# Kernel optimization log

Measured on AMD Instinct MI355X. Metric: run time of the kernel, lower is better.

The kernel has to match this reference:

```python
import jax, jax.numpy as jnp
import numpy as np


def setup_inputs() -> dict:
    key = jax.random.key(0)
    kx, kz = jax.random.split(key)
    B, H, W = 4, 512, 2048
    x = jax.random.normal(kx, (B, 1, H, W), dtype=jnp.float32)
    z = jax.random.uniform(kz, (B, 1, H, W), dtype=jnp.float32)
    return {"x": x, "z": z, "w_ceil": 16}


def reference(x, z, w_ceil):
    # The two structured sparse conv2d's reduce exactly to:
    #   z_exp[b,i,h,j] = z[b,0,h,j-i]            (eye_filter: right-shift, zero pad)
    #   out[b,i,h,j]   = (x*z_exp)[b,i,h,j+i]    (delay kernel + slice: left-shift, zero pad)
    # => out[b,i,h,j] = x[b,0,h,j+i] * z[b,0,h,j], zero where j+i >= W.
    B, _, H, W = x.shape
    shifts = jnp.arange(w_ceil)                       # [w]
    idx = jnp.arange(W)[None, :] + shifts[:, None]    # [w, W], value j+i
    valid = (idx < W)[None, :, None, :]               # [1, w, 1, W]
    idx = jnp.minimum(idx, W - 1)                     # clamp, masked below
    xg = jnp.take(x[:, 0], idx, axis=-1)              # [B, H, w, W]
    xg = jnp.transpose(xg, (0, 2, 1, 3))              # [B, w, H, W]
    out = jnp.where(valid, xg * z, jnp.zeros((), x.dtype))  # z broadcasts over channel dim
    return out
```

## Files before the change

kernel.cpp:

```cpp
#include <hip/hip_runtime.h>


#define B_ 4
#define H_ 512
#define W_ 2048
#define WC_ 16

__global__ __launch_bounds__(256) void
space2features_kernel(const float* __restrict__ x,
                      const float* __restrict__ z,
                      float* __restrict__ out) {
    const int blk = blockIdx.x;
    const int h = blk & (H_ - 1);
    const int i = (blk >> 9) & (WC_ - 1);
    const int b = blk >> 13;

    const size_t inrow = ((size_t)(b * H_ + h)) * W_;
    const float* __restrict__ xr = x + inrow;
    const float* __restrict__ zr = z + inrow;
    float* __restrict__ orow = out + (size_t)blk * W_;

    const int t = threadIdx.x;
    const int ibase = i & ~3;
    const int r = i & 3;
    const bool last_row = (b == B_ - 1) && (h == H_ - 1);

#pragma unroll
    for (int half = 0; half < 2; ++half) {
        const int j = half * 1024 + t * 4;
        const float4 z4 = *(const float4*)(zr + j);
        const int ji = j + i;

        float w0, w1, w2, w3;
        if (!last_row) {
            const float4 A = *(const float4*)(xr + j + ibase);
            const float4 Bv = *(const float4*)(xr + j + ibase + 4);
            switch (r) {
                case 0:  w0 = A.x; w1 = A.y; w2 = A.z; w3 = A.w; break;
                case 1:  w0 = A.y; w1 = A.z; w2 = A.w; w3 = Bv.x; break;
                case 2:  w0 = A.z; w1 = A.w; w2 = Bv.x; w3 = Bv.y; break;
                default: w0 = A.w; w1 = Bv.x; w2 = Bv.y; w3 = Bv.z; break;
            }
        } else {
            w0 = xr[min(ji + 0, W_ - 1)];
            w1 = xr[min(ji + 1, W_ - 1)];
            w2 = xr[min(ji + 2, W_ - 1)];
            w3 = xr[min(ji + 3, W_ - 1)];
        }

        float4 o;
        o.x = (ji + 0 < W_) ? w0 * z4.x : 0.0f;
        o.y = (ji + 1 < W_) ? w1 * z4.y : 0.0f;
        o.z = (ji + 2 < W_) ? w2 * z4.z : 0.0f;
        o.w = (ji + 3 < W_) ? w3 * z4.w : 0.0f;
        *(float4*)(orow + j) = o;
    }
}

extern "C" void kernel_launch(void* const* d_in, const int* in_sizes, int n_in,
                              void* d_out, int out_size, void* d_ws, size_t ws_size,
                              hipStream_t stream) {
    const float* x = (const float*)d_in[0];
    const float* z = (const float*)d_in[1];
    float* out = (float*)d_out;

    const int grid = B_ * WC_ * H_;
    space2features_kernel<<<grid, 256, 0, stream>>>(x, z, out);
}
```

Measured before the change: 290.0 us.

## Stage x row in LDS and emit all 16 shifts per block

Each block now handles one (b,h) row. It loads x and z once, stages x in shared memory with a zero-padded tail, and writes all 16 shifted output channels from registers. This removes the 16x redundant global reads of x and z and the per-block shift switch, and zero padding replaces the bounds masks. The grid shrinks 16x, which may cut parallelism and latency hiding. Each thread also issues 16 strided stores.

```diff
diff --git a/kernel.cpp b/kernel.cpp
--- a/kernel.cpp
+++ b/kernel.cpp
@@ -10,50 +10,50 @@
 space2features_kernel(const float* __restrict__ x,
                       const float* __restrict__ z,
                       float* __restrict__ out) {
+    __shared__ float xs[W_ + 20];
+
     const int blk = blockIdx.x;
     const int h = blk & (H_ - 1);
-    const int i = (blk >> 9) & (WC_ - 1);
-    const int b = blk >> 13;
+    const int b = blk >> 9;
 
-    const size_t inrow = ((size_t)(b * H_ + h)) * W_;
+    const size_t inrow = (size_t)blk * W_;
     const float* __restrict__ xr = x + inrow;
     const float* __restrict__ zr = z + inrow;
-    float* __restrict__ orow = out + (size_t)blk * W_;
 
     const int t = threadIdx.x;
-    const int ibase = i & ~3;
-    const int r = i & 3;
-    const bool last_row = (b == B_ - 1) && (h == H_ - 1);
+
+    float4 zv[2];
+#pragma unroll
+    for (int half = 0; half < 2; ++half) {
+        const int j = half * 1024 + t * 4;
+        const float4 x4 = *(const float4*)(xr + j);
+        zv[half] = *(const float4*)(zr + j);
+        *(float4*)(xs + j) = x4;
+    }
+    if (t < 20) xs[W_ + t] = 0.0f;
+    __syncthreads();
+
+    float* __restrict__ obase = out + ((size_t)(b * WC_) * H_ + h) * W_;
 
 #pragma unroll
     for (int half = 0; half < 2; ++half) {
         const int j = half * 1024 + t * 4;
-        const float4 z4 = *(const float4*)(zr + j);
-        const int ji = j + i;
 
-        float w0, w1, w2, w3;
-        if (!last_row) {
-            const float4 A = *(const float4*)(xr + j + ibase);
-            const float4 Bv = *(const float4*)(xr + j + ibase + 4);
-            switch (r) {
-                case 0:  w0 = A.x; w1 = A.y; w2 = A.z; w3 = A.w; break;
-                case 1:  w0 = A.y; w1 = A.z; w2 = A.w; w3 = Bv.x; break;
-                case 2:  w0 = A.z; w1 = A.w; w2 = Bv.x; w3 = Bv.y; break;
-                default: w0 = A.w; w1 = Bv.x; w2 = Bv.y; w3 = Bv.z; break;
-            }
-        } else {
-            w0 = xr[min(ji + 0, W_ - 1)];
-            w1 = xr[min(ji + 1, W_ - 1)];
-            w2 = xr[min(ji + 2, W_ - 1)];
-            w3 = xr[min(ji + 3, W_ - 1)];
+        float xv[20];
+#pragma unroll
+        for (int g = 0; g < 5; ++g)
+            *(float4*)(xv + 4 * g) = *(const float4*)(xs + j + 4 * g);
+
+        const float4 z4 = zv[half];
+#pragma unroll
+        for (int i = 0; i < WC_; ++i) {
+            float4 o;
+            o.x = xv[i + 0] * z4.x;
+            o.y = xv[i + 1] * z4.y;
+            o.z = xv[i + 2] * z4.z;
+            o.w = xv[i + 3] * z4.w;
+            *(float4*)(obase + (size_t)i * (H_ * W_) + j) = o;
         }
-
-        float4 o;
-        o.x = (ji + 0 < W_) ? w0 * z4.x : 0.0f;
-        o.y = (ji + 1 < W_) ? w1 * z4.y : 0.0f;
-        o.z = (ji + 2 < W_) ? w2 * z4.z : 0.0f;
-        o.w = (ji + 3 < W_) ? w3 * z4.w : 0.0f;
-        *(float4*)(orow + j) = o;
     }
 }
 
@@ -64,6 +64,6 @@
     const float* z = (const float*)d_in[1];
     float* out = (float*)d_out;
 
-    const int grid = B_ * WC_ * H_;
+    const int grid = B_ * H_;
     space2features_kernel<<<grid, 256, 0, stream>>>(x, z, out);
 }
```

Measured after the change: 300.2 us. 1.04x slower.
